# Optimization experiments

Measured on AMD Instinct MI355X. Metric: run time of the kernel, lower is better.

Reference implementation:

```python
import jax, jax.numpy as jnp
import numpy as np

B, C, N = 8, 64, 4096
K, M = 20, 8  # neighbors, num_kernel
OUT_C = 64
NEG_SLOPE = 0.2


def setup_inputs() -> dict:
    key = jax.random.key(0)
    k1, k2, k3, k4, k5, k6 = jax.random.split(key, 6)
    x = jax.random.normal(k1, (B, 3, N), dtype=jnp.float32)
    feature = jax.random.normal(k2, (B, C, N), dtype=jnp.float32)
    neigh_indexs = jax.random.randint(k3, (B, N, K), 0, N, dtype=jnp.int64)
    kernels = jax.random.normal(k4, (3, M), dtype=jnp.float32)
    conv_w = jax.random.normal(k5, (OUT_C, C * M), dtype=jnp.float32) * (1.0 / np.sqrt(C * M))
    conv_b = jax.random.normal(k6, (OUT_C,), dtype=jnp.float32) * 0.01
    return {"x": x, "feature": feature, "neigh_indexs": neigh_indexs,
            "kernels": kernels, "conv_w": conv_w, "conv_b": conv_b}


def reference(x, feature, neigh_indexs, kernels, conv_w, conv_b):
    b, c, n = feature.shape
    k = K
    m = kernels.shape[1]
    idx = neigh_indexs[:, :, :k]  # dilation=1 slice, (B,N,K)
    bidx = jnp.arange(b)[:, None, None]

    xt = jnp.transpose(x, (0, 2, 1))            # (B,N,3)
    x_neighs = xt[bidx, idx]                    # (B,N,K,3) irregular gather
    x_rel = x_neighs - x_neighs[:, :, :1, :]    # relative coords to first neighbor

    # kernel projection + one_padding buffer (zeros with [0,0]=1)
    one_pad = jnp.zeros((k, m), dtype=x.dtype).at[0, 0].set(1.0)
    permatrix = jnp.einsum('bnkc,cm->bnkm', x_rel, kernels) + one_pad
    # topkmax: stable softmax over the neighbor axis (soft assignment of
    # neighbors to each of the m kernel slots)
    permatrix = jax.nn.softmax(permatrix, axis=2)  # (B,N,K,M)

    ft = jnp.transpose(feature, (0, 2, 1))      # (B,N,C)
    f_neighs = ft[bidx, idx]                    # (B,N,K,C)
    # feats (B*N,C,K) @ permatrix (B*N,K,M) -> (B*N,C,M); flatten C-major
    agg = jnp.einsum('bnkc,bnkm->bncm', f_neighs, permatrix).reshape(b, n, c * m)

    # BasicConv: 1x1 conv == dense over channel dim, then LeakyReLU(0.2)
    out = agg @ conv_w.T + conv_b               # (B,N,out_c)
    out = jax.nn.leaky_relu(out, NEG_SLOPE)
    out = jnp.transpose(out, (0, 2, 1))         # (B,out_c,N)
    return out + feature                        # residual since in_c == out_c
```

## Files before the change

kernel.cpp:

```cpp
#include <hip/hip_runtime.h>

#define BB 8
#define CC 64
#define NNN 4096
#define KK 20
#define MM 8
#define OC 64
#define CM 512

typedef __attribute__((ext_vector_type(8))) short bf16x8;
typedef __attribute__((ext_vector_type(4))) float f32x4;

__device__ __forceinline__ unsigned short f2bf(float f) {
    union { float f; unsigned int u; } v; v.f = f;
    unsigned int u = v.u;
    return (unsigned short)((u + 0x7FFFu + ((u >> 16) & 1u)) >> 16);
}
__device__ __forceinline__ float bfhi2f(unsigned int u) {
    union { unsigned int u; float f; } v; v.u = u & 0xffff0000u; return v.f;
}
__device__ __forceinline__ float bflo2f(unsigned int u) {
    union { unsigned int u; float f; } v; v.u = u << 16; return v.f;
}

__global__ __launch_bounds__(256) void prep_kernel(const float* __restrict__ feature,
                                                   const float* __restrict__ conv_w,
                                                   unsigned short* __restrict__ ftr,
                                                   unsigned short* __restrict__ Wb) {
    int blk = blockIdx.x;
    int t = threadIdx.x;
    if (blk < 512) {
        __shared__ float tile[64 * 65];
        int b = blk & 7;
        int n0 = (blk >> 3) << 6;
        const float* fb = feature + b * (CC * NNN);
        #pragma unroll
        for (int s = 0; s < 16; ++s) {
            int i = t + s * 256;
            int c = i >> 6, nn = i & 63;
            tile[c * 65 + nn] = fb[c * NNN + n0 + nn];
        }
        __syncthreads();
        unsigned short* fo = ftr + b * (NNN * CC) + n0 * CC;
        #pragma unroll
        for (int s = 0; s < 16; ++s) {
            int i = t + s * 256;
            int n = i >> 6, cc = i & 63;
            fo[n * CC + cc] = f2bf(tile[cc * 65 + n]);
        }
    } else {
        int base = (blk - 512) * 8192;
        #pragma unroll
        for (int s = 0; s < 32; ++s) {
            int i = base + t + s * 256;
            Wb[i] = f2bf(conv_w[i]);
        }
    }
}

__global__ __launch_bounds__(256) void main_kernel(
    const float* __restrict__ x,
    const float* __restrict__ feature,
    const int* __restrict__ nidx,
    const float* __restrict__ kern,
    const float* __restrict__ conv_b,
    const unsigned short* __restrict__ ftr,
    const unsigned short* __restrict__ Wb,
    float* __restrict__ out)
{
    __shared__ int idx_lds[16 * KK];
    __shared__ float xn_lds[16 * KK * 3];
    __shared__ __align__(16) float perm_lds[16 * KK * MM];
    __shared__ __align__(16) unsigned short aggA[16 * 520];

    int t = threadIdx.x;
    int blk = blockIdx.x;
    int b = blk & 7;
    int n0 = (blk >> 3) << 4;

    const int* nb = nidx + (b * NNN + n0) * KK;
    for (int i = t; i < 16 * KK; i += 256) idx_lds[i] = nb[i];
    __syncthreads();

    const float* xb = x + b * (3 * NNN);
    for (int i = t; i < 16 * KK * 3; i += 256) {
        int p = i / 60;
        int rem = i - p * 60;
        int k = rem / 3;
        int c = rem - k * 3;
        xn_lds[i] = xb[c * NNN + idx_lds[p * KK + k]];
    }
    __syncthreads();

    if (t < 128) {
        int p = t >> 3;
        int m = t & 7;
        float k0 = kern[0 * MM + m], k1 = kern[1 * MM + m], k2 = kern[2 * MM + m];
        const float* xp = &xn_lds[p * 60];
        float bx = xp[0], by = xp[1], bz = xp[2];
        float pv[KK];
        #pragma unroll
        for (int k = 0; k < KK; ++k) {
            float dx = xp[k * 3 + 0] - bx;
            float dy = xp[k * 3 + 1] - by;
            float dz = xp[k * 3 + 2] - bz;
            pv[k] = dx * k0 + dy * k1 + dz * k2;
        }
        if (m == 0) pv[0] += 1.0f;
        float mx = pv[0];
        #pragma unroll
        for (int k = 1; k < KK; ++k) mx = fmaxf(mx, pv[k]);
        float sum = 0.f;
        #pragma unroll
        for (int k = 0; k < KK; ++k) { pv[k] = __expf(pv[k] - mx); sum += pv[k]; }
        float inv = 1.0f / sum;
        #pragma unroll
        for (int k = 0; k < KK; ++k) perm_lds[(p * KK + k) * MM + m] = pv[k] * inv;
    }
    __syncthreads();

    {
        int p = t >> 4;
        int cq = (t & 15) << 2;
        const unsigned short* fb = ftr + (size_t)b * (NNN * CC);
        float acc[4][MM];
        #pragma unroll
        for (int ci = 0; ci < 4; ++ci)
            #pragma unroll
            for (int m = 0; m < MM; ++m) acc[ci][m] = 0.f;
        int idxr[KK];
        #pragma unroll
        for (int k = 0; k < KK; ++k) idxr[k] = idx_lds[p * KK + k];
        #pragma unroll
        for (int k = 0; k < KK; ++k) {
            uint2 rv = *(const uint2*)(fb + idxr[k] * CC + cq);
            float fv[4];
            fv[0] = bflo2f(rv.x); fv[1] = bfhi2f(rv.x);
            fv[2] = bflo2f(rv.y); fv[3] = bfhi2f(rv.y);
            float4 pm0 = *(const float4*)&perm_lds[(p * KK + k) * MM];
            float4 pm1 = *(const float4*)&perm_lds[(p * KK + k) * MM + 4];
            float pvv[8] = {pm0.x, pm0.y, pm0.z, pm0.w, pm1.x, pm1.y, pm1.z, pm1.w};
            #pragma unroll
            for (int ci = 0; ci < 4; ++ci)
                #pragma unroll
                for (int m = 0; m < MM; ++m)
                    acc[ci][m] += fv[ci] * pvv[m];
        }
        #pragma unroll
        for (int ci = 0; ci < 4; ++ci) {
            union { bf16x8 v; unsigned short s[8]; } u;
            #pragma unroll
            for (int m = 0; m < MM; ++m) u.s[m] = f2bf(acc[ci][m]);
            *(bf16x8*)&aggA[p * 520 + (cq + ci) * MM] = u.v;
        }
    }
    __syncthreads();

    {
        int w = t >> 6;
        int l = t & 63;
        int o0 = w << 4;
        int row = l & 15;
        int kg = (l >> 4) << 3;
        f32x4 acc = {0.f, 0.f, 0.f, 0.f};
        const unsigned short* wrow = Wb + (o0 + row) * CM;
        const unsigned short* arow = aggA + row * 520;
        #pragma unroll
        for (int s = 0; s < 16; ++s) {
            int k = s * 32 + kg;
            bf16x8 af = *(const bf16x8*)&arow[k];
            bf16x8 bfr = *(const bf16x8*)&wrow[k];
            acc = __builtin_amdgcn_mfma_f32_16x16x32_bf16(af, bfr, acc, 0, 0, 0);
        }
        int o = o0 + row;
        float bias = conv_b[o];
        const float* fres = feature + b * (CC * NNN) + o * NNN + n0;
        float* op = out + b * (OC * NNN) + o * NNN + n0;
        #pragma unroll
        for (int r = 0; r < 4; ++r) {
            int pt = ((l >> 4) << 2) + r;
            float v = acc[r] + bias;
            v = v > 0.f ? v : v * 0.2f;
            op[pt] = v + fres[pt];
        }
    }
}

extern "C" void kernel_launch(void* const* d_in, const int* in_sizes, int n_in,
                              void* d_out, int out_size, void* d_ws, size_t ws_size,
                              hipStream_t stream) {
    const float* x        = (const float*)d_in[0];
    const float* feature  = (const float*)d_in[1];
    const int*   nidx     = (const int*)d_in[2];
    const float* kern     = (const float*)d_in[3];
    const float* conv_w   = (const float*)d_in[4];
    const float* conv_b   = (const float*)d_in[5];
    float* out = (float*)d_out;

    unsigned short* ftr = (unsigned short*)d_ws;
    unsigned short* Wb  = (unsigned short*)((char*)d_ws + 4194304);

    prep_kernel<<<516, 256, 0, stream>>>(feature, conv_w, ftr, Wb);
    main_kernel<<<2048, 256, 0, stream>>>(x, feature, nidx, kern, conv_b, ftr, Wb, out);
}
```

Before: 109.7 us.

## Prefetch neighbor features early, alias LDS buffers, and vectorize epilogue stores

Moves the bf16 neighbor-feature gathers, residual load, bias and kernel weights before the softmax stage so their global-memory latency overlaps with the coordinate gather and softmax compute. LDS is shrunk by putting the early-stage buffers and the aggregation tile in a union, and perm rows are padded to stride 10. A launch-bounds occupancy hint is added and the output is written as float4. Holding 20 prefetched uint2 values in registers raises register pressure, and the LDS aliasing needs an extra barrier.

```diff
diff --git a/kernel.cpp b/kernel.cpp
--- a/kernel.cpp
+++ b/kernel.cpp
@@ -58,7 +58,7 @@
     }
 }
 
-__global__ __launch_bounds__(256) void main_kernel(
+__global__ __launch_bounds__(256, 4) void main_kernel(
     const float* __restrict__ x,
     const float* __restrict__ feature,
     const int* __restrict__ nidx,
@@ -68,35 +68,65 @@
     const unsigned short* __restrict__ Wb,
     float* __restrict__ out)
 {
-    __shared__ int idx_lds[16 * KK];
-    __shared__ float xn_lds[16 * KK * 3];
-    __shared__ __align__(16) float perm_lds[16 * KK * MM];
-    __shared__ __align__(16) unsigned short aggA[16 * 520];
+    __shared__ __align__(16) union {
+        struct {
+            int   idx[16 * KK];
+            float xn[16 * KK * 3];
+            float perm[16 * KK * 10];
+        } s;
+        unsigned short aggA[16 * 520];
+    } u;
 
     int t = threadIdx.x;
     int blk = blockIdx.x;
     int b = blk & 7;
     int n0 = (blk >> 3) << 4;
+    int w = t >> 6, l = t & 63;
+
+    int o = (w << 4) + (l & 15);
+    int pq = (l >> 4) << 2;
+    float4 fres4 = *(const float4*)(feature + ((size_t)b * CC + o) * NNN + n0 + pq);
+    float bias = conv_b[o];
+    int m_pre = t & 7;
+    float kw0 = kern[m_pre], kw1 = kern[MM + m_pre], kw2 = kern[2 * MM + m_pre];
 
     const int* nb = nidx + (b * NNN + n0) * KK;
-    for (int i = t; i < 16 * KK; i += 256) idx_lds[i] = nb[i];
+    for (int i = t; i < 16 * KK; i += 256) u.s.idx[i] = nb[i];
     __syncthreads();
 
     const float* xb = x + b * (3 * NNN);
-    for (int i = t; i < 16 * KK * 3; i += 256) {
-        int p = i / 60;
-        int rem = i - p * 60;
-        int k = rem / 3;
-        int c = rem - k * 3;
-        xn_lds[i] = xb[c * NNN + idx_lds[p * KK + k]];
-    }
+    float xreg[4];
+    int xslot[4];
+    #pragma unroll
+    for (int s = 0; s < 4; ++s) {
+        int i = t + s * 256;
+        xslot[s] = i;
+        if (i < 960) {
+            int p2 = i / 60;
+            int rem = i - p2 * 60;
+            int k = rem / 3;
+            int c = rem - k * 3;
+            xreg[s] = xb[c * NNN + u.s.idx[p2 * KK + k]];
+        }
+    }
+
+    int p = t >> 4;
+    int cq = (t & 15) << 2;
+    const unsigned short* fb = ftr + (size_t)b * (NNN * CC);
+    uint2 fr[KK];
+    #pragma unroll
+    for (int k = 0; k < KK; ++k)
+        fr[k] = *(const uint2*)(fb + (size_t)u.s.idx[p * KK + k] * CC + cq);
+
+    #pragma unroll
+    for (int s = 0; s < 4; ++s)
+        if (xslot[s] < 960) u.s.xn[xslot[s]] = xreg[s];
     __syncthreads();
 
     if (t < 128) {
-        int p = t >> 3;
+        int pp = t >> 3;
         int m = t & 7;
-        float k0 = kern[0 * MM + m], k1 = kern[1 * MM + m], k2 = kern[2 * MM + m];
-        const float* xp = &xn_lds[p * 60];
+        const float* xp = &u.s.xn[pp * 60];
         float bx = xp[0], by = xp[1], bz = xp[2];
         float pv[KK];
         #pragma unroll
@@ -104,7 +134,7 @@
             float dx = xp[k * 3 + 0] - bx;
             float dy = xp[k * 3 + 1] - by;
             float dz = xp[k * 3 + 2] - bz;
-            pv[k] = dx * k0 + dy * k1 + dz * k2;
+            pv[k] = dx * kw0 + dy * kw1 + dz * kw2;
         }
         if (m == 0) pv[0] += 1.0f;
         float mx = pv[0];
@@ -115,74 +145,64 @@
         for (int k = 0; k < KK; ++k) { pv[k] = __expf(pv[k] - mx); sum += pv[k]; }
         float inv = 1.0f / sum;
         #pragma unroll
-        for (int k = 0; k < KK; ++k) perm_lds[(p * KK + k) * MM + m] = pv[k] * inv;
-    }
-    __syncthreads();
-
-    {
-        int p = t >> 4;
-        int cq = (t & 15) << 2;
-        const unsigned short* fb = ftr + (size_t)b * (NNN * CC);
-        float acc[4][MM];
+        for (int k = 0; k < KK; ++k) u.s.perm[(pp * KK + k) * 10 + m] = pv[k] * inv;
+    }
+    __syncthreads();
+
+    float acc[4][MM];
+    #pragma unroll
+    for (int ci = 0; ci < 4; ++ci)
+        #pragma unroll
+        for (int m = 0; m < MM; ++m) acc[ci][m] = 0.f;
+    #pragma unroll
+    for (int k = 0; k < KK; ++k) {
+        float fv[4];
+        fv[0] = bflo2f(fr[k].x); fv[1] = bfhi2f(fr[k].x);
+        fv[2] = bflo2f(fr[k].y); fv[3] = bfhi2f(fr[k].y);
+        const float* pr = &u.s.perm[(p * KK + k) * 10];
+        float2 q0 = *(const float2*)(pr + 0);
+        float2 q1 = *(const float2*)(pr + 2);
+        float2 q2 = *(const float2*)(pr + 4);
+        float2 q3 = *(const float2*)(pr + 6);
+        float pvv[8] = {q0.x, q0.y, q1.x, q1.y, q2.x, q2.y, q3.x, q3.y};
         #pragma unroll
         for (int ci = 0; ci < 4; ++ci)
             #pragma unroll
-            for (int m = 0; m < MM; ++m) acc[ci][m] = 0.f;
-        int idxr[KK];
-        #pragma unroll
-        for (int k = 0; k < KK; ++k) idxr[k] = idx_lds[p * KK + k];
-        #pragma unroll
-        for (int k = 0; k < KK; ++k) {
-            uint2 rv = *(const uint2*)(fb + idxr[k] * CC + cq);
-            float fv[4];
-            fv[0] = bflo2f(rv.x); fv[1] = bfhi2f(rv.x);
-            fv[2] = bflo2f(rv.y); fv[3] = bfhi2f(rv.y);
-            float4 pm0 = *(const float4*)&perm_lds[(p * KK + k) * MM];
-            float4 pm1 = *(const float4*)&perm_lds[(p * KK + k) * MM + 4];
-            float pvv[8] = {pm0.x, pm0.y, pm0.z, pm0.w, pm1.x, pm1.y, pm1.z, pm1.w};
-            #pragma unroll
-            for (int ci = 0; ci < 4; ++ci)
-                #pragma unroll
-                for (int m = 0; m < MM; ++m)
-                    acc[ci][m] += fv[ci] * pvv[m];
-        }
-        #pragma unroll
-        for (int ci = 0; ci < 4; ++ci) {
-            union { bf16x8 v; unsigned short s[8]; } u;
-            #pragma unroll
-            for (int m = 0; m < MM; ++m) u.s[m] = f2bf(acc[ci][m]);
-            *(bf16x8*)&aggA[p * 520 + (cq + ci) * MM] = u.v;
-        }
+            for (int m = 0; m < MM; ++m)
+                acc[ci][m] += fv[ci] * pvv[m];
+    }
+    __syncthreads();
+
+    #pragma unroll
+    for (int ci = 0; ci < 4; ++ci) {
+        union { bf16x8 v; unsigned short s2[8]; } pk;
+        #pragma unroll
+        for (int m = 0; m < MM; ++m) pk.s2[m] = f2bf(acc[ci][m]);
+        *(bf16x8*)&u.aggA[p * 520 + (cq + ci) * MM] = pk.v;
     }
     __syncthreads();
 
     {
-        int w = t >> 6;
-        int l = t & 63;
-        int o0 = w << 4;
         int row = l & 15;
         int kg = (l >> 4) << 3;
-        f32x4 acc = {0.f, 0.f, 0.f, 0.f};
-        const unsigned short* wrow = Wb + (o0 + row) * CM;
-        const unsigned short* arow = aggA + row * 520;
+        f32x4 acc2 = {0.f, 0.f, 0.f, 0.f};
+        const unsigned short* wrow = Wb + (size_t)o * CM;
+        const unsigned short* arow = u.aggA + row * 520;
         #pragma unroll
         for (int s = 0; s < 16; ++s) {
             int k = s * 32 + kg;
             bf16x8 af = *(const bf16x8*)&arow[k];
             bf16x8 bfr = *(const bf16x8*)&wrow[k];
-            acc = __builtin_amdgcn_mfma_f32_16x16x32_bf16(af, bfr, acc, 0, 0, 0);
-        }
-        int o = o0 + row;
-        float bias = conv_b[o];
-        const float* fres = feature + b * (CC * NNN) + o * NNN + n0;
-        float* op = out + b * (OC * NNN) + o * NNN + n0;
+            acc2 = __builtin_amdgcn_mfma_f32_16x16x32_bf16(af, bfr, acc2, 0, 0, 0);
+        }
+        float4 res;
         #pragma unroll
         for (int r = 0; r < 4; ++r) {
-            int pt = ((l >> 4) << 2) + r;
-            float v = acc[r] + bias;
+            float v = acc2[r] + bias;
             v = v > 0.f ? v : v * 0.2f;
-            op[pt] = v + fres[pt];
-        }
+            ((float*)&res)[r] = v + ((const float*)&fres4)[r];
+        }
+        *(float4*)(out + ((size_t)b * CC + o) * NNN + n0 + pq) = res;
     }
 }
 
```

Measured after the change: 106.7 us. 2.7% less time.

## Restructure main kernel to 128 threads with per-wave regions and prefetched gathers

Applied to the files above, without the earlier changes.

Shrinks the main kernel block to two waves, each owning eight points with a private LDS region that reuses the same memory for coordinates, softmax weights and bf16 aggregate. Neighbor feature rows are gathered as 16-byte vectors and double-buffered in registers, overlapping the gather latency with the weighted accumulation, which now uses packed float2 math. The GEMM stage has each wave compute two 16x16 output tiles and emit float4 stores with vectorized residual loads. The aim is to hide gather latency and cut synchronization and store traffic, at the cost of higher register pressure under launch bounds of 128 threads with 3 blocks per SM.

```diff
diff --git a/kernel.cpp b/kernel.cpp
--- a/kernel.cpp
+++ b/kernel.cpp
@@ -1,4 +1,5 @@
 #include <hip/hip_runtime.h>
+#include <hip/hip_bf16.h>
 
 #define BB 8
 #define CC 64
@@ -7,14 +8,22 @@
 #define MM 8
 #define OC 64
 #define CM 512
+#define AST 516
+#define REGB 8352
 
 typedef __attribute__((ext_vector_type(8))) short bf16x8;
 typedef __attribute__((ext_vector_type(4))) float f32x4;
+typedef __attribute__((ext_vector_type(2))) float f32x2;
 
 __device__ __forceinline__ unsigned short f2bf(float f) {
     union { float f; unsigned int u; } v; v.f = f;
     unsigned int u = v.u;
     return (unsigned short)((u + 0x7FFFu + ((u >> 16) & 1u)) >> 16);
+}
+__device__ __forceinline__ unsigned int pack2bf(float a, float b) {
+    union { __hip_bfloat162 h; unsigned int u; } pk;
+    pk.h = __float22bfloat162_rn(make_float2(a, b));
+    return pk.u;
 }
 __device__ __forceinline__ float bfhi2f(unsigned int u) {
     union { unsigned int u; float f; } v; v.u = u & 0xffff0000u; return v.f;
@@ -58,7 +67,7 @@
     }
 }
 
-__global__ __launch_bounds__(256) void main_kernel(
+__global__ __launch_bounds__(128, 3) void main_kernel(
     const float* __restrict__ x,
     const float* __restrict__ feature,
     const int* __restrict__ nidx,
@@ -68,43 +77,64 @@
     const unsigned short* __restrict__ Wb,
     float* __restrict__ out)
 {
-    __shared__ int idx_lds[16 * KK];
-    __shared__ float xn_lds[16 * KK * 3];
-    __shared__ __align__(16) float perm_lds[16 * KK * MM];
-    __shared__ __align__(16) unsigned short aggA[16 * 520];
+    __shared__ __align__(16) unsigned char smem[2 * REGB];
 
     int t = threadIdx.x;
+    int w = t >> 6, l = t & 63;
     int blk = blockIdx.x;
     int b = blk & 7;
     int n0 = (blk >> 3) << 4;
 
-    const int* nb = nidx + (b * NNN + n0) * KK;
-    for (int i = t; i < 16 * KK; i += 256) idx_lds[i] = nb[i];
-    __syncthreads();
-
+    float* xnF  = (float*)(smem + w * REGB);
+    float* permF = xnF + 480;
+
+    int p = l >> 3;
+    int m = l & 7;
+    int cL = l & 7;
+
+    const int* nb_w = nidx + ((b * NNN + n0 + w * 8)) * KK;
     const float* xb = x + b * (3 * NNN);
-    for (int i = t; i < 16 * KK * 3; i += 256) {
-        int p = i / 60;
-        int rem = i - p * 60;
-        int k = rem / 3;
-        int c = rem - k * 3;
-        xn_lds[i] = xb[c * NNN + idx_lds[p * KK + k]];
-    }
-    __syncthreads();
-
-    if (t < 128) {
-        int p = t >> 3;
-        int m = t & 7;
-        float k0 = kern[0 * MM + m], k1 = kern[1 * MM + m], k2 = kern[2 * MM + m];
-        const float* xp = &xn_lds[p * 60];
-        float bx = xp[0], by = xp[1], bz = xp[2];
+    const unsigned short* fbb = ftr + (size_t)b * (NNN * CC);
+
+    const int4* nb4 = (const int4*)(nb_w + p * KK);
+    int4 idc0 = nb4[0];
+    int4 idc1 = nb4[1];
+    float kw0 = kern[m], kw1 = kern[MM + m], kw2 = kern[2 * MM + m];
+
+    #pragma unroll
+    for (int s = 0; s < 8; ++s) {
+        int i = l + s * 64;
+        if (i < 480) {
+            int p2 = i / 60;
+            int rem = i - p2 * 60;
+            int k = rem / 3;
+            int c = rem - k * 3;
+            int idv = nb_w[p2 * KK + k];
+            xnF[i] = xb[c * NNN + idv];
+        }
+    }
+
+    uint4 frA[4], frB[4];
+    {
+        const int* ic = (const int*)&idc0;
+        #pragma unroll
+        for (int j = 0; j < 4; ++j)
+            frA[j] = *(const uint4*)(fbb + (size_t)ic[j] * CC + cL * 8);
+    }
+    __syncthreads();
+
+    {
+        const float* xp = xnF + p * 60;
         float pv[KK];
-        #pragma unroll
-        for (int k = 0; k < KK; ++k) {
-            float dx = xp[k * 3 + 0] - bx;
-            float dy = xp[k * 3 + 1] - by;
-            float dz = xp[k * 3 + 2] - bz;
-            pv[k] = dx * k0 + dy * k1 + dz * k2;
+        float bx, by, bz;
+        #pragma unroll
+        for (int tt = 0; tt < 10; ++tt) {
+            f32x2 a = *(const f32x2*)(xp + 6 * tt);
+            f32x2 bq = *(const f32x2*)(xp + 6 * tt + 2);
+            f32x2 cq = *(const f32x2*)(xp + 6 * tt + 4);
+            if (tt == 0) { bx = a.x; by = a.y; bz = bq.x; }
+            pv[2 * tt]     = (a.x - bx) * kw0 + (a.y - by) * kw1 + (bq.x - bz) * kw2;
+            pv[2 * tt + 1] = (bq.y - bx) * kw0 + (cq.x - by) * kw1 + (cq.y - bz) * kw2;
         }
         if (m == 0) pv[0] += 1.0f;
         float mx = pv[0];
@@ -115,74 +145,114 @@
         for (int k = 0; k < KK; ++k) { pv[k] = __expf(pv[k] - mx); sum += pv[k]; }
         float inv = 1.0f / sum;
         #pragma unroll
-        for (int k = 0; k < KK; ++k) perm_lds[(p * KK + k) * MM + m] = pv[k] * inv;
-    }
-    __syncthreads();
-
-    {
-        int p = t >> 4;
-        int cq = (t & 15) << 2;
-        const unsigned short* fb = ftr + (size_t)b * (NNN * CC);
-        float acc[4][MM];
-        #pragma unroll
-        for (int ci = 0; ci < 4; ++ci)
+        for (int k = 0; k < KK; ++k) permF[(p * KK + k) * 10 + m] = pv[k] * inv;
+    }
+    __syncthreads();
+
+    f32x2 accp[4][MM];
+    #pragma unroll
+    for (int cp = 0; cp < 4; ++cp)
+        #pragma unroll
+        for (int mm2 = 0; mm2 < MM; ++mm2) accp[cp][mm2] = (f32x2){0.f, 0.f};
+
+    int4 idnext = idc1;
+    #pragma unroll
+    for (int c4 = 0; c4 < 5; ++c4) {
+        uint4* cur = (c4 & 1) ? frB : frA;
+        uint4* nxt = (c4 & 1) ? frA : frB;
+        if (c4 < 4) {
+            const int* in_ = (const int*)&idnext;
             #pragma unroll
-            for (int m = 0; m < MM; ++m) acc[ci][m] = 0.f;
-        int idxr[KK];
-        #pragma unroll
-        for (int k = 0; k < KK; ++k) idxr[k] = idx_lds[p * KK + k];
-        #pragma unroll
-        for (int k = 0; k < KK; ++k) {
-            uint2 rv = *(const uint2*)(fb + idxr[k] * CC + cq);
-            float fv[4];
-            fv[0] = bflo2f(rv.x); fv[1] = bfhi2f(rv.x);
-            fv[2] = bflo2f(rv.y); fv[3] = bfhi2f(rv.y);
-            float4 pm0 = *(const float4*)&perm_lds[(p * KK + k) * MM];
-            float4 pm1 = *(const float4*)&perm_lds[(p * KK + k) * MM + 4];
-            float pvv[8] = {pm0.x, pm0.y, pm0.z, pm0.w, pm1.x, pm1.y, pm1.z, pm1.w};
+            for (int j = 0; j < 4; ++j)
+                nxt[j] = *(const uint4*)(fbb + (size_t)in_[j] * CC + cL * 8);
+        }
+        if (c4 < 3) idnext = nb4[c4 + 2];
+        #pragma unroll
+        for (int j = 0; j < 4; ++j) {
+            int k = c4 * 4 + j;
+            const float* pr = permF + (p * KK + k) * 10;
+            f32x2 pm0 = *(const f32x2*)(pr + 0);
+            f32x2 pm1 = *(const f32x2*)(pr + 2);
+            f32x2 pm2 = *(const f32x2*)(pr + 4);
+            f32x2 pm3 = *(const f32x2*)(pr + 6);
+            float pms[8] = {pm0.x, pm0.y, pm1.x, pm1.y, pm2.x, pm2.y, pm3.x, pm3.y};
+            const unsigned int* dw = (const unsigned int*)&cur[j];
+            f32x2 fvp[4];
             #pragma unroll
-            for (int ci = 0; ci < 4; ++ci)
+            for (int d = 0; d < 4; ++d)
+                fvp[d] = (f32x2){bflo2f(dw[d]), bfhi2f(dw[d])};
+            #pragma unroll
+            for (int mm2 = 0; mm2 < MM; ++mm2) {
+                f32x2 pmm = {pms[mm2], pms[mm2]};
                 #pragma unroll
-                for (int m = 0; m < MM; ++m)
-                    acc[ci][m] += fv[ci] * pvv[m];
-        }
-        #pragma unroll
-        for (int ci = 0; ci < 4; ++ci) {
-            union { bf16x8 v; unsigned short s[8]; } u;
-            #pragma unroll
-            for (int m = 0; m < MM; ++m) u.s[m] = f2bf(acc[ci][m]);
-            *(bf16x8*)&aggA[p * 520 + (cq + ci) * MM] = u.v;
-        }
-    }
-    __syncthreads();
-
-    {
-        int w = t >> 6;
-        int l = t & 63;
-        int o0 = w << 4;
-        int row = l & 15;
-        int kg = (l >> 4) << 3;
-        f32x4 acc = {0.f, 0.f, 0.f, 0.f};
-        const unsigned short* wrow = Wb + (o0 + row) * CM;
-        const unsigned short* arow = aggA + row * 520;
+                for (int cp = 0; cp < 4; ++cp)
+                    accp[cp][mm2] += fvp[cp] * pmm;
+            }
+        }
+    }
+    __syncthreads();
+
+    {
+        unsigned short* aggRow = (unsigned short*)(smem + w * REGB) + p * AST + cL * 8 * MM;
+        #pragma unroll
+        for (int i = 0; i < 8; ++i) {
+            int cp = i >> 1;
+            unsigned int d0, d1, d2, d3;
+            if ((i & 1) == 0) {
+                d0 = pack2bf(accp[cp][0].x, accp[cp][1].x);
+                d1 = pack2bf(accp[cp][2].x, accp[cp][3].x);
+                d2 = pack2bf(accp[cp][4].x, accp[cp][5].x);
+                d3 = pack2bf(accp[cp][6].x, accp[cp][7].x);
+            } else {
+                d0 = pack2bf(accp[cp][0].y, accp[cp][1].y);
+                d1 = pack2bf(accp[cp][2].y, accp[cp][3].y);
+                d2 = pack2bf(accp[cp][4].y, accp[cp][5].y);
+                d3 = pack2bf(accp[cp][6].y, accp[cp][7].y);
+            }
+            uint2* dst = (uint2*)(aggRow + i * MM);
+            dst[0] = make_uint2(d0, d1);
+            dst[1] = make_uint2(d2, d3);
+        }
+    }
+    __syncthreads();
+
+    {
+        int o0 = w * 32 + (l & 15);
+        int o1 = o0 + 16;
+        int q = l >> 4;
+        int rowp = l & 15;
+        const unsigned short* arow = (const unsigned short*)(smem + (rowp >> 3) * REGB)
+                                     + (rowp & 7) * AST + q * 8;
+        const unsigned short* wr0 = Wb + (size_t)o0 * CM + q * 8;
+        const unsigned short* wr1 = Wb + (size_t)o1 * CM + q * 8;
+        const float* fbase = feature + (size_t)b * (CC * NNN) + n0 + q * 4;
+        float4 res0 = *(const float4*)(fbase + (size_t)o0 * NNN);
+        float4 res1 = *(const float4*)(fbase + (size_t)o1 * NNN);
+        float bias0 = conv_b[o0], bias1 = conv_b[o1];
+
+        f32x4 d0 = {0.f, 0.f, 0.f, 0.f};
+        f32x4 d1 = {0.f, 0.f, 0.f, 0.f};
         #pragma unroll
         for (int s = 0; s < 16; ++s) {
-            int k = s * 32 + kg;
-            bf16x8 af = *(const bf16x8*)&arow[k];
-            bf16x8 bfr = *(const bf16x8*)&wrow[k];
-            acc = __builtin_amdgcn_mfma_f32_16x16x32_bf16(af, bfr, acc, 0, 0, 0);
-        }
-        int o = o0 + row;
-        float bias = conv_b[o];
-        const float* fres = feature + b * (CC * NNN) + o * NNN + n0;
-        float* op = out + b * (OC * NNN) + o * NNN + n0;
+            bf16x8 af = *(const bf16x8*)(arow + s * 32);
+            bf16x8 b0 = *(const bf16x8*)(wr0 + s * 32);
+            bf16x8 b1 = *(const bf16x8*)(wr1 + s * 32);
+            d0 = __builtin_amdgcn_mfma_f32_16x16x32_bf16(af, b0, d0, 0, 0, 0);
+            d1 = __builtin_amdgcn_mfma_f32_16x16x32_bf16(af, b1, d1, 0, 0, 0);
+        }
+        float* ob = out + (size_t)b * (OC * NNN) + n0 + q * 4;
+        float4 r0, r1;
         #pragma unroll
         for (int r = 0; r < 4; ++r) {
-            int pt = ((l >> 4) << 2) + r;
-            float v = acc[r] + bias;
-            v = v > 0.f ? v : v * 0.2f;
-            op[pt] = v + fres[pt];
-        }
+            float v0 = d0[r] + bias0;
+            v0 = v0 > 0.f ? v0 : v0 * 0.2f;
+            ((float*)&r0)[r] = v0 + ((const float*)&res0)[r];
+            float v1 = d1[r] + bias1;
+            v1 = v1 > 0.f ? v1 : v1 * 0.2f;
+            ((float*)&r1)[r] = v1 + ((const float*)&res1)[r];
+        }
+        *(float4*)(ob + (size_t)o0 * NNN) = r0;
+        *(float4*)(ob + (size_t)o1 * NNN) = r1;
     }
 }
 
@@ -201,5 +271,5 @@
     unsigned short* Wb  = (unsigned short*)((char*)d_ws + 4194304);
 
     prep_kernel<<<516, 256, 0, stream>>>(feature, conv_w, ftr, Wb);
-    main_kernel<<<2048, 256, 0, stream>>>(x, feature, nidx, kern, conv_b, ftr, Wb, out);
-}
+    main_kernel<<<2048, 128, 0, stream>>>(x, feature, nidx, kern, conv_b, ftr, Wb, out);
+}
```

Result: no change. 110.5 us (+0.8%).

## Split main kernel into aggregation and GEMM kernels with precomputed projections

Applied to the files above, without the earlier changes.

The softmax logits are rewritten using linearity: each point's coordinates are projected onto the kernels once in the prep kernel, and each neighbor's logit becomes a gathered projection minus the first neighbor's. This removes the per-neighbor xyz gather and recompute. The fused main kernel is split into a per-wave aggregation kernel that writes bf16 aggregates to a global buffer, plus a separate MFMA GEMM kernel with a 32x32 tile per wave. The weight columns are permuted to match the new aggregate layout. In exchange the intermediate aggregate goes through a round trip in global memory and there is an extra kernel launch.

```diff
diff --git a/kernel.cpp b/kernel.cpp
--- a/kernel.cpp
+++ b/kernel.cpp
@@ -1,4 +1,5 @@
 #include <hip/hip_runtime.h>
+#include <hip/hip_bf16.h>
 
 #define BB 8
 #define CC 64
@@ -10,12 +11,18 @@
 
 typedef __attribute__((ext_vector_type(8))) short bf16x8;
 typedef __attribute__((ext_vector_type(4))) float f32x4;
+typedef __attribute__((ext_vector_type(2))) float f32x2;
 
 __device__ __forceinline__ unsigned short f2bf(float f) {
     union { float f; unsigned int u; } v; v.f = f;
     unsigned int u = v.u;
     return (unsigned short)((u + 0x7FFFu + ((u >> 16) & 1u)) >> 16);
 }
+__device__ __forceinline__ unsigned int pack2bf(float a, float b) {
+    union { __hip_bfloat162 h; unsigned int u; } pk;
+    pk.h = __float22bfloat162_rn(make_float2(a, b));
+    return pk.u;
+}
 __device__ __forceinline__ float bfhi2f(unsigned int u) {
     union { unsigned int u; float f; } v; v.u = u & 0xffff0000u; return v.f;
 }
@@ -23,10 +30,13 @@
     union { unsigned int u; float f; } v; v.u = u << 16; return v.f;
 }
 
-__global__ __launch_bounds__(256) void prep_kernel(const float* __restrict__ feature,
+__global__ __launch_bounds__(256) void prep_kernel(const float* __restrict__ x,
+                                                   const float* __restrict__ feature,
+                                                   const float* __restrict__ kern,
                                                    const float* __restrict__ conv_w,
                                                    unsigned short* __restrict__ ftr,
-                                                   unsigned short* __restrict__ Wb) {
+                                                   unsigned short* __restrict__ Wb,
+                                                   float* __restrict__ proj) {
     int blk = blockIdx.x;
     int t = threadIdx.x;
     if (blk < 512) {
@@ -48,142 +58,205 @@
             int n = i >> 6, cc = i & 63;
             fo[n * CC + cc] = f2bf(tile[cc * 65 + n]);
         }
-    } else {
+    } else if (blk < 516) {
         int base = (blk - 512) * 8192;
         #pragma unroll
         for (int s = 0; s < 32; ++s) {
             int i = base + t + s * 256;
-            Wb[i] = f2bf(conv_w[i]);
-        }
-    }
-}
-
-__global__ __launch_bounds__(256) void main_kernel(
-    const float* __restrict__ x,
-    const float* __restrict__ feature,
-    const int* __restrict__ nidx,
-    const float* __restrict__ kern,
-    const float* __restrict__ conv_b,
-    const unsigned short* __restrict__ ftr,
-    const unsigned short* __restrict__ Wb,
-    float* __restrict__ out)
-{
-    __shared__ int idx_lds[16 * KK];
-    __shared__ float xn_lds[16 * KK * 3];
-    __shared__ __align__(16) float perm_lds[16 * KK * MM];
-    __shared__ __align__(16) unsigned short aggA[16 * 520];
-
-    int t = threadIdx.x;
+            int o = i >> 9, col = i & 511;
+            int j = col >> 6, cL = (col >> 3) & 7, m = col & 7;
+            int cm = ((cL * 8 + j) << 3) | m;
+            Wb[i] = f2bf(conv_w[(o << 9) | cm]);
+        }
+    } else {
+        int pb = blk - 516;
+        int b = pb >> 2;
+        int nb = (pb & 3) << 10;
+        const float* xb = x + b * (3 * NNN);
+        float k0[MM], k1[MM], k2[MM];
+        #pragma unroll
+        for (int m = 0; m < MM; ++m) {
+            k0[m] = kern[m]; k1[m] = kern[MM + m]; k2[m] = kern[2 * MM + m];
+        }
+        #pragma unroll
+        for (int s = 0; s < 4; ++s) {
+            int n = nb + s * 256 + t;
+            float x0 = xb[n], x1 = xb[NNN + n], x2 = xb[2 * NNN + n];
+            float pr[MM];
+            #pragma unroll
+            for (int m = 0; m < MM; ++m)
+                pr[m] = x0 * k0[m] + x1 * k1[m] + x2 * k2[m];
+            float* pp = proj + ((size_t)b * NNN + n) * MM;
+            *(float4*)pp = make_float4(pr[0], pr[1], pr[2], pr[3]);
+            *(float4*)(pp + 4) = make_float4(pr[4], pr[5], pr[6], pr[7]);
+        }
+    }
+}
+
+__global__ __launch_bounds__(256, 3) void aggr_kernel(const int* __restrict__ nidx,
+                                                      const float* __restrict__ proj,
+                                                      const unsigned short* __restrict__ ftr,
+                                                      unsigned short* __restrict__ agg) {
+    __shared__ unsigned short perm[4][8 * 168];
+
+    int t = threadIdx.x, w = t >> 6, l = t & 63;
+    int p = l >> 3, h = l & 7;
     int blk = blockIdx.x;
     int b = blk & 7;
-    int n0 = (blk >> 3) << 4;
-
-    const int* nb = nidx + (b * NNN + n0) * KK;
-    for (int i = t; i < 16 * KK; i += 256) idx_lds[i] = nb[i];
-    __syncthreads();
-
-    const float* xb = x + b * (3 * NNN);
-    for (int i = t; i < 16 * KK * 3; i += 256) {
-        int p = i / 60;
-        int rem = i - p * 60;
-        int k = rem / 3;
-        int c = rem - k * 3;
-        xn_lds[i] = xb[c * NNN + idx_lds[p * KK + k]];
-    }
-    __syncthreads();
-
-    if (t < 128) {
-        int p = t >> 3;
-        int m = t & 7;
-        float k0 = kern[0 * MM + m], k1 = kern[1 * MM + m], k2 = kern[2 * MM + m];
-        const float* xp = &xn_lds[p * 60];
-        float bx = xp[0], by = xp[1], bz = xp[2];
-        float pv[KK];
-        #pragma unroll
-        for (int k = 0; k < KK; ++k) {
-            float dx = xp[k * 3 + 0] - bx;
-            float dy = xp[k * 3 + 1] - by;
-            float dz = xp[k * 3 + 2] - bz;
-            pv[k] = dx * k0 + dy * k1 + dz * k2;
-        }
-        if (m == 0) pv[0] += 1.0f;
-        float mx = pv[0];
-        #pragma unroll
-        for (int k = 1; k < KK; ++k) mx = fmaxf(mx, pv[k]);
-        float sum = 0.f;
-        #pragma unroll
-        for (int k = 0; k < KK; ++k) { pv[k] = __expf(pv[k] - mx); sum += pv[k]; }
-        float inv = 1.0f / sum;
-        #pragma unroll
-        for (int k = 0; k < KK; ++k) perm_lds[(p * KK + k) * MM + m] = pv[k] * inv;
-    }
-    __syncthreads();
-
+    int n0 = ((blk >> 3) << 5) + (w << 3);
+    int rowp = b * NNN + n0 + p;
+
+    int id[KK];
     {
-        int p = t >> 4;
-        int cq = (t & 15) << 2;
-        const unsigned short* fb = ftr + (size_t)b * (NNN * CC);
-        float acc[4][MM];
-        #pragma unroll
-        for (int ci = 0; ci < 4; ++ci)
+        const int4* nb4 = (const int4*)(nidx + rowp * KK);
+        #pragma unroll
+        for (int s = 0; s < 5; ++s) {
+            int4 v = nb4[s];
+            id[s * 4 + 0] = v.x; id[s * 4 + 1] = v.y;
+            id[s * 4 + 2] = v.z; id[s * 4 + 3] = v.w;
+        }
+    }
+
+    const float* pj = proj + (size_t)b * NNN * MM;
+    float pv[KK];
+    #pragma unroll
+    for (int k = 0; k < KK; ++k) pv[k] = pj[id[k] * MM + h];
+
+    const unsigned short* fb = ftr + (size_t)b * NNN * CC;
+    uint4 fr[KK];
+    #pragma unroll
+    for (int k = 0; k < KK; ++k)
+        fr[k] = *(const uint4*)(fb + (size_t)id[k] * CC + h * 8);
+
+    float pbase = pv[0];
+    #pragma unroll
+    for (int k = 0; k < KK; ++k) pv[k] -= pbase;
+    if (h == 0) pv[0] += 1.0f;
+    float mx = pv[0];
+    #pragma unroll
+    for (int k = 1; k < KK; ++k) mx = fmaxf(mx, pv[k]);
+    float sum = 0.f;
+    #pragma unroll
+    for (int k = 0; k < KK; ++k) { pv[k] = __expf(pv[k] - mx); sum += pv[k]; }
+    float inv = 1.0f / sum;
+
+    {
+        unsigned short* pw = perm[w] + p * 168;
+        #pragma unroll
+        for (int k = 0; k < KK; ++k) pw[k * 8 + h] = f2bf(pv[k] * inv);
+    }
+    __asm__ __volatile__("s_waitcnt lgkmcnt(0)" ::: "memory");
+
+    f32x2 acc[4][MM];
+    #pragma unroll
+    for (int d = 0; d < 4; ++d)
+        #pragma unroll
+        for (int m = 0; m < MM; ++m) acc[d][m] = (f32x2){0.f, 0.f};
+
+    const unsigned short* prd = perm[w] + p * 168;
+    #pragma unroll
+    for (int k = 0; k < KK; ++k) {
+        union { bf16x8 v; unsigned int u[4]; } pm8;
+        pm8.v = *(const bf16x8*)(prd + k * 8);
+        float pm[MM];
+        #pragma unroll
+        for (int d = 0; d < 4; ++d) {
+            pm[2 * d] = bflo2f(pm8.u[d]);
+            pm[2 * d + 1] = bfhi2f(pm8.u[d]);
+        }
+        const unsigned int* fu = (const unsigned int*)&fr[k];
+        f32x2 fv[4];
+        #pragma unroll
+        for (int d = 0; d < 4; ++d)
+            fv[d] = (f32x2){bflo2f(fu[d]), bfhi2f(fu[d])};
+        #pragma unroll
+        for (int m = 0; m < MM; ++m) {
+            f32x2 pmm = {pm[m], pm[m]};
             #pragma unroll
-            for (int m = 0; m < MM; ++m) acc[ci][m] = 0.f;
-        int idxr[KK];
-        #pragma unroll
-        for (int k = 0; k < KK; ++k) idxr[k] = idx_lds[p * KK + k];
-        #pragma unroll
-        for (int k = 0; k < KK; ++k) {
-            uint2 rv = *(const uint2*)(fb + idxr[k] * CC + cq);
-            float fv[4];
-            fv[0] = bflo2f(rv.x); fv[1] = bfhi2f(rv.x);
-            fv[2] = bflo2f(rv.y); fv[3] = bfhi2f(rv.y);
-            float4 pm0 = *(const float4*)&perm_lds[(p * KK + k) * MM];
-            float4 pm1 = *(const float4*)&perm_lds[(p * KK + k) * MM + 4];
-            float pvv[8] = {pm0.x, pm0.y, pm0.z, pm0.w, pm1.x, pm1.y, pm1.z, pm1.w};
-            #pragma unroll
-            for (int ci = 0; ci < 4; ++ci)
-                #pragma unroll
-                for (int m = 0; m < MM; ++m)
-                    acc[ci][m] += fv[ci] * pvv[m];
-        }
-        #pragma unroll
-        for (int ci = 0; ci < 4; ++ci) {
-            union { bf16x8 v; unsigned short s[8]; } u;
-            #pragma unroll
-            for (int m = 0; m < MM; ++m) u.s[m] = f2bf(acc[ci][m]);
-            *(bf16x8*)&aggA[p * 520 + (cq + ci) * MM] = u.v;
-        }
-    }
-    __syncthreads();
-
-    {
-        int w = t >> 6;
-        int l = t & 63;
-        int o0 = w << 4;
-        int row = l & 15;
-        int kg = (l >> 4) << 3;
-        f32x4 acc = {0.f, 0.f, 0.f, 0.f};
-        const unsigned short* wrow = Wb + (o0 + row) * CM;
-        const unsigned short* arow = aggA + row * 520;
-        #pragma unroll
-        for (int s = 0; s < 16; ++s) {
-            int k = s * 32 + kg;
-            bf16x8 af = *(const bf16x8*)&arow[k];
-            bf16x8 bfr = *(const bf16x8*)&wrow[k];
-            acc = __builtin_amdgcn_mfma_f32_16x16x32_bf16(af, bfr, acc, 0, 0, 0);
-        }
-        int o = o0 + row;
-        float bias = conv_b[o];
-        const float* fres = feature + b * (CC * NNN) + o * NNN + n0;
-        float* op = out + b * (OC * NNN) + o * NNN + n0;
-        #pragma unroll
-        for (int r = 0; r < 4; ++r) {
-            int pt = ((l >> 4) << 2) + r;
-            float v = acc[r] + bias;
-            v = v > 0.f ? v : v * 0.2f;
-            op[pt] = v + fres[pt];
-        }
-    }
+            for (int d = 0; d < 4; ++d)
+                acc[d][m] += fv[d] * pmm;
+        }
+    }
+
+    unsigned short* ag = agg + (size_t)rowp * CM;
+    #pragma unroll
+    for (int jj = 0; jj < 8; ++jj) {
+        int d = jj >> 1;
+        unsigned int d0, d1, d2, d3;
+        if ((jj & 1) == 0) {
+            d0 = pack2bf(acc[d][0].x, acc[d][1].x);
+            d1 = pack2bf(acc[d][2].x, acc[d][3].x);
+            d2 = pack2bf(acc[d][4].x, acc[d][5].x);
+            d3 = pack2bf(acc[d][6].x, acc[d][7].x);
+        } else {
+            d0 = pack2bf(acc[d][0].y, acc[d][1].y);
+            d1 = pack2bf(acc[d][2].y, acc[d][3].y);
+            d2 = pack2bf(acc[d][4].y, acc[d][5].y);
+            d3 = pack2bf(acc[d][6].y, acc[d][7].y);
+        }
+        uint4 vv = make_uint4(d0, d1, d2, d3);
+        *(uint4*)(ag + jj * 64 + h * 8) = vv;
+    }
+}
+
+__global__ __launch_bounds__(128, 4) void gemm_kernel(const unsigned short* __restrict__ agg,
+                                                      const unsigned short* __restrict__ Wb,
+                                                      const float* __restrict__ conv_b,
+                                                      const float* __restrict__ feature,
+                                                      float* __restrict__ out) {
+    int t = threadIdx.x, w = t >> 6, l = t & 63;
+    int blk = blockIdx.x;
+    int b = blk & 7;
+    int g = blk >> 3;
+    int Wid = g * 2 + w;
+    int og = Wid & 1;
+    int pg = Wid >> 1;
+    int n0 = pg << 5;
+    int oA = og * 32 + (l & 15), oB = oA + 16;
+    int q = l >> 4;
+    int r0 = b * NNN + n0 + (l & 15);
+
+    const unsigned short* a0p = agg + (size_t)r0 * CM + q * 8;
+    const unsigned short* a1p = a0p + 16 * CM;
+    const unsigned short* w0p = Wb + (size_t)oA * CM + q * 8;
+    const unsigned short* w1p = Wb + (size_t)oB * CM + q * 8;
+
+    const float* fA = feature + ((size_t)b * CC + oA) * NNN + n0 + q * 4;
+    const float* fB = feature + ((size_t)b * CC + oB) * NNN + n0 + q * 4;
+    float4 resA0 = *(const float4*)fA;
+    float4 resA1 = *(const float4*)(fA + 16);
+    float4 resB0 = *(const float4*)fB;
+    float4 resB1 = *(const float4*)(fB + 16);
+    float biasA = conv_b[oA], biasB = conv_b[oB];
+
+    f32x4 d00 = {0,0,0,0}, d01 = {0,0,0,0}, d10 = {0,0,0,0}, d11 = {0,0,0,0};
+    #pragma unroll
+    for (int s = 0; s < 16; ++s) {
+        bf16x8 a0 = *(const bf16x8*)(a0p + s * 32);
+        bf16x8 a1 = *(const bf16x8*)(a1p + s * 32);
+        bf16x8 w0f = *(const bf16x8*)(w0p + s * 32);
+        bf16x8 w1f = *(const bf16x8*)(w1p + s * 32);
+        d00 = __builtin_amdgcn_mfma_f32_16x16x32_bf16(a0, w0f, d00, 0, 0, 0);
+        d01 = __builtin_amdgcn_mfma_f32_16x16x32_bf16(a0, w1f, d01, 0, 0, 0);
+        d10 = __builtin_amdgcn_mfma_f32_16x16x32_bf16(a1, w0f, d10, 0, 0, 0);
+        d11 = __builtin_amdgcn_mfma_f32_16x16x32_bf16(a1, w1f, d11, 0, 0, 0);
+    }
+
+    float* opA = out + ((size_t)b * OC + oA) * NNN + n0 + q * 4;
+    float* opB = out + ((size_t)b * OC + oB) * NNN + n0 + q * 4;
+    float4 rA0, rA1, rB0, rB1;
+    #pragma unroll
+    for (int r = 0; r < 4; ++r) {
+        float v;
+        v = d00[r] + biasA; v = v > 0.f ? v : v * 0.2f; ((float*)&rA0)[r] = v + ((const float*)&resA0)[r];
+        v = d10[r] + biasA; v = v > 0.f ? v : v * 0.2f; ((float*)&rA1)[r] = v + ((const float*)&resA1)[r];
+        v = d01[r] + biasB; v = v > 0.f ? v : v * 0.2f; ((float*)&rB0)[r] = v + ((const float*)&resB0)[r];
+        v = d11[r] + biasB; v = v > 0.f ? v : v * 0.2f; ((float*)&rB1)[r] = v + ((const float*)&resB1)[r];
+    }
+    *(float4*)opA = rA0;
+    *(float4*)(opA + 16) = rA1;
+    *(float4*)opB = rB0;
+    *(float4*)(opB + 16) = rB1;
 }
 
 extern "C" void kernel_launch(void* const* d_in, const int* in_sizes, int n_in,
@@ -197,9 +270,13 @@
     const float* conv_b   = (const float*)d_in[5];
     float* out = (float*)d_out;
 
-    unsigned short* ftr = (unsigned short*)d_ws;
-    unsigned short* Wb  = (unsigned short*)((char*)d_ws + 4194304);
-
-    prep_kernel<<<516, 256, 0, stream>>>(feature, conv_w, ftr, Wb);
-    main_kernel<<<2048, 256, 0, stream>>>(x, feature, nidx, kern, conv_b, ftr, Wb, out);
-}
+    char* ws = (char*)d_ws;
+    unsigned short* ftr  = (unsigned short*)ws;
+    unsigned short* Wb   = (unsigned short*)(ws + (4u << 20));
+    float*          proj = (float*)(ws + (4u << 20) + (64u << 10));
+    unsigned short* agg  = (unsigned short*)(ws + (5u << 20) + (64u << 10));
+
+    prep_kernel<<<548, 256, 0, stream>>>(x, feature, kern, conv_w, ftr, Wb, proj);
+    aggr_kernel<<<1024, 256, 0, stream>>>(nidx, proj, ftr, agg);
+    gemm_kernel<<<1024, 128, 0, stream>>>(agg, Wb, conv_b, feature, out);
+}
```

New measurement: 120.1 us. 9.5% more time.
